# Kernel optimization log

Measured on AMD Instinct MI355X. Metric: run time of the kernel, lower is better.

Reference implementation:

```python
import jax, jax.numpy as jnp
import numpy as np

N_NODES = 20000
N_EDGES = 320000
IN_F = 256
OUT_F = 256
EDGE_F = 256


def _mlp2(x, W1, b1, W2, b2):
    # MLPLayers(2, [d_in, 2*d_in, d_out]) = Linear -> ReLU -> Linear
    return jax.nn.relu(x @ W1 + b1) @ W2 + b2


def setup_inputs() -> dict:
    key = jax.random.key(0)
    ks = jax.random.split(key, 12)

    def lin(k, fan_in, shape):
        bound = 1.0 / np.sqrt(fan_in)
        return jax.random.uniform(k, shape, jnp.float32, -bound, bound)

    node_feat = jax.random.normal(ks[0], (N_NODES, IN_F), jnp.float32)
    edge_feat = jax.random.normal(ks[1], (N_EDGES, EDGE_F), jnp.float32)
    src = jax.random.randint(ks[2], (N_EDGES,), 0, N_NODES, jnp.int32)
    dst = jax.random.randint(ks[3], (N_EDGES,), 0, N_NODES, jnp.int32)

    # edge_mlp: edge_feats -> 2*edge_feats -> in_feats
    We1 = lin(ks[4], EDGE_F, (EDGE_F, 2 * EDGE_F))
    be1 = lin(ks[5], EDGE_F, (2 * EDGE_F,))
    We2 = lin(ks[6], 2 * EDGE_F, (2 * EDGE_F, IN_F))
    be2 = lin(ks[7], 2 * EDGE_F, (IN_F,))
    # node mlp: in_feats -> 2*in_feats -> out_feats
    Wn1 = lin(ks[8], IN_F, (IN_F, 2 * IN_F))
    bn1 = lin(ks[9], IN_F, (2 * IN_F,))
    Wn2 = lin(ks[10], 2 * IN_F, (2 * IN_F, OUT_F))
    bn2 = lin(ks[11], 2 * IN_F, (OUT_F,))
    eps = jnp.zeros((1,), jnp.float32)

    return {"node_feat": node_feat, "edge_feat": edge_feat, "src": src, "dst": dst,
            "We1": We1, "be1": be1, "We2": We2, "be2": be2,
            "Wn1": Wn1, "bn1": bn1, "Wn2": Wn2, "bn2": bn2, "eps": eps}


def reference(node_feat, edge_feat, src, dst, We1, be1, We2, be2, Wn1, bn1, Wn2, bn2, eps):
    e = _mlp2(edge_feat, We1, be1, We2, be2)            # [E, IN_F]
    msg = jax.nn.relu(node_feat[src] + e)               # gather-add-relu
    out_h = jax.ops.segment_sum(msg, dst, num_segments=N_NODES)  # [N, IN_F]
    out = _mlp2((1.0 + eps[0]) * node_feat + out_h, Wn1, bn1, Wn2, bn2)
    return out
```

## Files before the change

kernel.cpp:

```cpp
#include <hip/hip_runtime.h>
#include <hip/hip_bf16.h>

#define NN  20000
#define NE  320000
#define FIN 256
#define FH  512

typedef __attribute__((ext_vector_type(8))) short bf16x8;
typedef __attribute__((ext_vector_type(4))) float f32x4;
typedef __attribute__((ext_vector_type(4))) unsigned short u16x4;
typedef __attribute__((ext_vector_type(4))) unsigned int u32x4;

static __device__ __forceinline__ unsigned short f2b(float f) {
    union { float f; unsigned int i; } v; v.f = f;
    return (unsigned short)((v.i + 0x7fffu + ((v.i >> 16) & 1u)) >> 16);
}
static __device__ __forceinline__ f32x4 mfma16(bf16x8 a, bf16x8 b, f32x4 c) {
    return __builtin_amdgcn_mfma_f32_16x16x32_bf16(a, b, c, 0, 0, 0);
}
static __device__ __forceinline__ unsigned int cvtpk(float lo, float hi) {
    union { __hip_bfloat162 h; unsigned int u; } v;
    v.h = __float22bfloat162_rn(float2{lo, hi});
    return v.u;
}
static __device__ __forceinline__ u16x4 pack4(float a, float b, float c, float d) {
    union { u16x4 s; unsigned int u[2]; } v;
    v.u[0] = cvtpk(a, b); v.u[1] = cvtpk(c, d);
    return v.s;
}
static __device__ __forceinline__ bf16x8 cvt8(f32x4 a, f32x4 b) {
    u32x4 t;
    t[0] = cvtpk(a[0], a[1]);
    t[1] = cvtpk(a[2], a[3]);
    t[2] = cvtpk(b[0], b[1]);
    t[3] = cvtpk(b[2], b[3]);
    return __builtin_bit_cast(bf16x8, t);
}

__global__ void prep_weights(const float* __restrict__ We1, const float* __restrict__ We2,
                             const float* __restrict__ Wn1, const float* __restrict__ Wn2,
                             unsigned short* __restrict__ W1F, unsigned short* __restrict__ W2F,
                             unsigned short* __restrict__ Wn1F, unsigned short* __restrict__ Wn2F) {
    const int b = blockIdx.x;
    const int m = b >> 8;
    const int f = b & 255;
    const float* src; unsigned short* dst; int N, K;
    if      (m == 0) { src = We1; dst = W1F;  N = 512; K = 256; }
    else if (m == 1) { src = We2; dst = W2F;  N = 256; K = 512; }
    else if (m == 2) { src = Wn1; dst = Wn1F; N = 512; K = 256; }
    else             { src = Wn2; dst = Wn2F; N = 256; K = 512; }
    const int KB  = K >> 5;
    const int nf  = f / KB, ks = f % KB;
    const int l   = threadIdx.x;
    const int quad = l >> 4, ln = l & 15;
    const int n  = nf * 16 + ln;
    const int k0 = ks * 32 + quad * 8;
    f32x4 a, c;
    #pragma unroll
    for (int j = 0; j < 4; ++j) {
        a[j] = src[(size_t)(k0 + j) * N + n];
        c[j] = src[(size_t)(k0 + 4 + j) * N + n];
    }
    *(bf16x8*)(dst + ((size_t)f * 64 + l) * 8) = cvt8(a, c);
}

__global__ void hist_dst(const int* __restrict__ dstI, int* __restrict__ cnt) {
    int e = blockIdx.x * 256 + threadIdx.x;
    if (e < NE) atomicAdd(&cnt[dstI[e]], 1);
}

__global__ void scan_excl(const int* __restrict__ cnt, int* __restrict__ cursor) {
    __shared__ int c[NN];
    __shared__ int s[1024];
    const int t = threadIdx.x;
    for (int i = t; i < NN; i += 1024) c[i] = cnt[i];
    __syncthreads();
    const int lo = t * 20;
    const int hi = (lo + 20 < NN) ? lo + 20 : NN;
    int sum = 0;
    for (int i = lo; i < hi; ++i) sum += c[i];
    s[t] = sum;
    __syncthreads();
    for (int off = 1; off < 1024; off <<= 1) {
        int v = (t >= off) ? s[t - off] : 0;
        __syncthreads();
        s[t] += v;
        __syncthreads();
    }
    int base = (t > 0) ? s[t - 1] : 0;
    for (int i = lo; i < hi; ++i) { int cv = c[i]; c[i] = base; base += cv; }
    __syncthreads();
    for (int i = t; i < NN; i += 1024) cursor[i] = c[i];
}

__global__ void scatter_perm(const int* __restrict__ dstI,
                             int* __restrict__ cursor, int* __restrict__ perm) {
    int e = blockIdx.x * 256 + threadIdx.x;
    if (e < NE) {
        int pos = atomicAdd(&cursor[dstI[e]], 1);
        perm[pos] = e;
    }
}

__global__ void __launch_bounds__(512, 4)
gine_edge(const float* __restrict__ edge_feat,
          const float* __restrict__ node_feat,
          const int* __restrict__ srcI,
          const int* __restrict__ dstI,
          const int* __restrict__ perm,
          const unsigned short* __restrict__ W1F,
          const float* __restrict__ b1,
          const unsigned short* __restrict__ W2F,
          const float* __restrict__ b2,
          float* __restrict__ out_h)
{
    __shared__ union {
        unsigned short Xs[64 * 264];
        unsigned short Hs[64 * 512];
        float          Msg[64 * 260];
    } sh;
    __shared__ int snS[64], dnS[64];

    const int tid  = threadIdx.x;
    const int wave = tid >> 6;
    const int lane = tid & 63;
    const int quad = lane >> 4;
    const int ln   = lane & 15;
    const int bs   = (blockIdx.x & 7) * 625 + (blockIdx.x >> 3);
    const int e0   = bs * 64;

    #pragma unroll
    for (int it = 0; it < 4; ++it) {
        const int chunk = tid + it * 512;
        const int row = chunk >> 5;
        const int c8  = (chunk & 31) << 3;
        const int e   = perm[e0 + row];
        const float* p = edge_feat + (size_t)e * FIN + c8;
        f32x4 o0 = *(const f32x4*)(p);
        f32x4 o1 = *(const f32x4*)(p + 4);
        *(bf16x8*)(&sh.Xs[row * 264 + c8]) = cvt8(o0, o1);
    }
    if (tid < 64) {
        const int e = perm[e0 + tid];
        snS[tid] = srcI[e];
        dnS[tid] = dstI[e];
    }
    __syncthreads();

    f32x4 zero4 = {0.f, 0.f, 0.f, 0.f};
    f32x4 acc1[4][4];
    #pragma unroll
    for (int nt = 0; nt < 4; ++nt)
        #pragma unroll
        for (int et = 0; et < 4; ++et) acc1[nt][et] = zero4;

    __builtin_amdgcn_s_setprio(1);
    #pragma unroll
    for (int ks = 0; ks < 8; ++ks) {
        bf16x8 w[4], x[4];
        #pragma unroll
        for (int nt = 0; nt < 4; ++nt)
            w[nt] = *(const bf16x8*)(W1F + (((wave * 4 + nt) * 8 + ks) * 64 + lane) * 8);
        #pragma unroll
        for (int et = 0; et < 4; ++et)
            x[et] = *(const bf16x8*)(&sh.Xs[(et * 16 + ln) * 264 + quad * 8 + ks * 32]);
        #pragma unroll
        for (int nt = 0; nt < 4; ++nt)
            #pragma unroll
            for (int et = 0; et < 4; ++et)
                acc1[nt][et] = mfma16(w[nt], x[et], acc1[nt][et]);
    }
    __builtin_amdgcn_s_setprio(0);
    __syncthreads();

    #pragma unroll
    for (int nt = 0; nt < 4; ++nt) {
        const int n0 = wave * 64 + nt * 16 + quad * 4;
        const f32x4 b4 = *(const f32x4*)(b1 + n0);
        #pragma unroll
        for (int et = 0; et < 4; ++et) {
            const int edge = et * 16 + ln;
            u16x4 p = pack4(fmaxf(acc1[nt][et][0] + b4[0], 0.f),
                            fmaxf(acc1[nt][et][1] + b4[1], 0.f),
                            fmaxf(acc1[nt][et][2] + b4[2], 0.f),
                            fmaxf(acc1[nt][et][3] + b4[3], 0.f));
            *(u16x4*)(&sh.Hs[(edge << 9) + (((n0 >> 3) ^ (edge & 7)) << 3) + (n0 & 7)]) = p;
        }
    }
    __syncthreads();

    f32x4 nfr[2][4];
    #pragma unroll
    for (int nt = 0; nt < 2; ++nt) {
        const int n0 = wave * 32 + nt * 16 + quad * 4;
        #pragma unroll
        for (int et = 0; et < 4; ++et) {
            const int sn = snS[et * 16 + ln];
            nfr[nt][et] = *(const f32x4*)(node_feat + (size_t)sn * FIN + n0);
        }
    }

    f32x4 acc2[2][4];
    #pragma unroll
    for (int nt = 0; nt < 2; ++nt)
        #pragma unroll
        for (int et = 0; et < 4; ++et) acc2[nt][et] = zero4;

    __builtin_amdgcn_s_setprio(1);
    #pragma unroll
    for (int ks = 0; ks < 16; ++ks) {
        const int kb = ks * 4 + quad;
        bf16x8 w[2], h[4];
        #pragma unroll
        for (int nt = 0; nt < 2; ++nt)
            w[nt] = *(const bf16x8*)(W2F + (((wave * 2 + nt) * 16 + ks) * 64 + lane) * 8);
        #pragma unroll
        for (int et = 0; et < 4; ++et) {
            const int edge = et * 16 + ln;
            h[et] = *(const bf16x8*)(&sh.Hs[(edge << 9) + ((kb ^ (edge & 7)) << 3)]);
        }
        #pragma unroll
        for (int nt = 0; nt < 2; ++nt)
            #pragma unroll
            for (int et = 0; et < 4; ++et)
                acc2[nt][et] = mfma16(w[nt], h[et], acc2[nt][et]);
    }
    __builtin_amdgcn_s_setprio(0);
    __syncthreads();

    #pragma unroll
    for (int nt = 0; nt < 2; ++nt) {
        const int n0 = wave * 32 + nt * 16 + quad * 4;
        const f32x4 b4 = *(const f32x4*)(b2 + n0);
        #pragma unroll
        for (int et = 0; et < 4; ++et) {
            const int edge = et * 16 + ln;
            f32x4 m;
            #pragma unroll
            for (int r = 0; r < 4; ++r)
                m[r] = fmaxf(nfr[nt][et][r] + acc2[nt][et][r] + b4[r], 0.f);
            *(f32x4*)(&sh.Msg[edge * 260 + n0]) = m;
        }
    }
    __syncthreads();

    {
        const int col  = tid & 255;
        const int half = tid >> 8;
        const int rA   = half * 32;
        const int dF = dnS[rA], dL = dnS[rA + 31];
        float run = sh.Msg[rA * 260 + col];
        int cur = dF;
        #pragma unroll 4
        for (int row = rA + 1; row < rA + 32; ++row) {
            const int d = dnS[row];
            if (d != cur) {
                if (cur == dF || cur == dL)
                    atomicAdd(&out_h[(size_t)cur * FIN + col], run);
                else
                    out_h[(size_t)cur * FIN + col] = run;
                run = 0.f;
                cur = d;
            }
            run += sh.Msg[row * 260 + col];
        }
        atomicAdd(&out_h[(size_t)cur * FIN + col], run);
    }
}

__global__ void __launch_bounds__(512, 4)
gine_node(const float* __restrict__ node_feat,
          const float* __restrict__ out_h,
          const unsigned short* __restrict__ W1F,
          const float* __restrict__ b1,
          const unsigned short* __restrict__ W2F,
          const float* __restrict__ b2,
          const float* __restrict__ eps,
          float* __restrict__ out)
{
    __shared__ union {
        unsigned short Xs[64 * 264];
        unsigned short Hs[64 * 512];
    } sh;

    const int tid  = threadIdx.x;
    const int wave = tid >> 6;
    const int lane = tid & 63;
    const int quad = lane >> 4;
    const int ln   = lane & 15;
    const int n0b  = blockIdx.x * 64;
    const float epsv = 1.0f + eps[0];

    #pragma unroll
    for (int it = 0; it < 4; ++it) {
        const int chunk = tid + it * 512;
        const int row = chunk >> 5;
        const int c8  = (chunk & 31) << 3;
        const int g   = n0b + row;
        bf16x8 pack = {0, 0, 0, 0, 0, 0, 0, 0};
        if (g < NN) {
            const float* pn = node_feat + (size_t)g * FIN + c8;
            const float* ph = out_h + (size_t)g * FIN + c8;
            f32x4 n0v = *(const f32x4*)(pn);
            f32x4 n1v = *(const f32x4*)(pn + 4);
            f32x4 h0v = *(const f32x4*)(ph);
            f32x4 h1v = *(const f32x4*)(ph + 4);
            f32x4 a, b;
            #pragma unroll
            for (int j = 0; j < 4; ++j) {
                a[j] = epsv * n0v[j] + h0v[j];
                b[j] = epsv * n1v[j] + h1v[j];
            }
            pack = cvt8(a, b);
        }
        *(bf16x8*)(&sh.Xs[row * 264 + c8]) = pack;
    }
    __syncthreads();

    f32x4 zero4 = {0.f, 0.f, 0.f, 0.f};
    f32x4 acc1[4][4];
    #pragma unroll
    for (int nt = 0; nt < 4; ++nt)
        #pragma unroll
        for (int et = 0; et < 4; ++et) acc1[nt][et] = zero4;

    __builtin_amdgcn_s_setprio(1);
    #pragma unroll
    for (int ks = 0; ks < 8; ++ks) {
        bf16x8 w[4], xv[4];
        #pragma unroll
        for (int nt = 0; nt < 4; ++nt)
            w[nt] = *(const bf16x8*)(W1F + (((wave * 4 + nt) * 8 + ks) * 64 + lane) * 8);
        #pragma unroll
        for (int et = 0; et < 4; ++et)
            xv[et] = *(const bf16x8*)(&sh.Xs[(et * 16 + ln) * 264 + quad * 8 + ks * 32]);
        #pragma unroll
        for (int nt = 0; nt < 4; ++nt)
            #pragma unroll
            for (int et = 0; et < 4; ++et)
                acc1[nt][et] = mfma16(w[nt], xv[et], acc1[nt][et]);
    }
    __builtin_amdgcn_s_setprio(0);
    __syncthreads();

    #pragma unroll
    for (int nt = 0; nt < 4; ++nt) {
        const int n0 = wave * 64 + nt * 16 + quad * 4;
        const f32x4 b4 = *(const f32x4*)(b1 + n0);
        #pragma unroll
        for (int et = 0; et < 4; ++et) {
            const int edge = et * 16 + ln;
            u16x4 p = pack4(fmaxf(acc1[nt][et][0] + b4[0], 0.f),
                            fmaxf(acc1[nt][et][1] + b4[1], 0.f),
                            fmaxf(acc1[nt][et][2] + b4[2], 0.f),
                            fmaxf(acc1[nt][et][3] + b4[3], 0.f));
            *(u16x4*)(&sh.Hs[(edge << 9) + (((n0 >> 3) ^ (edge & 7)) << 3) + (n0 & 7)]) = p;
        }
    }
    __syncthreads();

    f32x4 acc2[2][4];
    #pragma unroll
    for (int nt = 0; nt < 2; ++nt)
        #pragma unroll
        for (int et = 0; et < 4; ++et) acc2[nt][et] = zero4;

    __builtin_amdgcn_s_setprio(1);
    #pragma unroll
    for (int ks = 0; ks < 16; ++ks) {
        const int kb = ks * 4 + quad;
        bf16x8 w[2], h[4];
        #pragma unroll
        for (int nt = 0; nt < 2; ++nt)
            w[nt] = *(const bf16x8*)(W2F + (((wave * 2 + nt) * 16 + ks) * 64 + lane) * 8);
        #pragma unroll
        for (int et = 0; et < 4; ++et) {
            const int edge = et * 16 + ln;
            h[et] = *(const bf16x8*)(&sh.Hs[(edge << 9) + ((kb ^ (edge & 7)) << 3)]);
        }
        #pragma unroll
        for (int nt = 0; nt < 2; ++nt)
            #pragma unroll
            for (int et = 0; et < 4; ++et)
                acc2[nt][et] = mfma16(w[nt], h[et], acc2[nt][et]);
    }
    __builtin_amdgcn_s_setprio(0);

    #pragma unroll
    for (int nt = 0; nt < 2; ++nt) {
        const int n0 = wave * 32 + nt * 16 + quad * 4;
        const f32x4 b4 = *(const f32x4*)(b2 + n0);
        #pragma unroll
        for (int et = 0; et < 4; ++et) {
            const int g = n0b + et * 16 + ln;
            if (g < NN) {
                f32x4 o;
                #pragma unroll
                for (int r = 0; r < 4; ++r)
                    o[r] = acc2[nt][et][r] + b4[r];
                *(f32x4*)(out + (size_t)g * FIN + n0) = o;
            }
        }
    }
}

extern "C" void kernel_launch(void* const* d_in, const int* in_sizes, int n_in,
                              void* d_out, int out_size, void* d_ws, size_t ws_size,
                              hipStream_t stream) {
    const float* node_feat = (const float*)d_in[0];
    const float* edge_feat = (const float*)d_in[1];
    const int* srcI = (const int*)d_in[2];
    const int* dstI = (const int*)d_in[3];
    const float* We1 = (const float*)d_in[4];
    const float* be1 = (const float*)d_in[5];
    const float* We2 = (const float*)d_in[6];
    const float* be2 = (const float*)d_in[7];
    const float* Wn1 = (const float*)d_in[8];
    const float* bn1 = (const float*)d_in[9];
    const float* Wn2 = (const float*)d_in[10];
    const float* bn2 = (const float*)d_in[11];
    const float* eps = (const float*)d_in[12];

    char* ws = (char*)d_ws;
    float* out_h = (float*)ws;
    unsigned short* W1F  = (unsigned short*)(ws + 20480000);
    unsigned short* W2F  = W1F + 131072;
    unsigned short* Wn1F = W2F + 131072;
    unsigned short* Wn2F = Wn1F + 131072;
    int* cnt    = (int*)(ws + 20480000 + 4 * 262144);
    int* cursor = cnt + NN;
    int* perm   = cursor + NN;

    hipMemsetAsync(out_h, 0, (size_t)NN * FIN * sizeof(float), stream);
    hipMemsetAsync(cnt, 0, NN * sizeof(int), stream);

    prep_weights<<<1024, 64, 0, stream>>>(We1, We2, Wn1, Wn2, W1F, W2F, Wn1F, Wn2F);

    hist_dst<<<(NE + 255) / 256, 256, 0, stream>>>(dstI, cnt);
    scan_excl<<<1, 1024, 0, stream>>>(cnt, cursor);
    scatter_perm<<<(NE + 255) / 256, 256, 0, stream>>>(dstI, cursor, perm);

    gine_edge<<<NE / 64, 512, 0, stream>>>(edge_feat, node_feat, srcI, dstI,
                                           perm, W1F, be1, W2F, be2, out_h);
    gine_node<<<(NN + 63) / 64, 512, 0, stream>>>(node_feat, out_h, Wn1F, bn1,
                                                  Wn2F, bn2, eps, (float*)d_out);
}
```

Measured before the change: 820.8 us.

## Overlap second half of edge-feature load with first-layer MFMA via async LDS loads

Splits the edge-feature tile load in the edge kernel into two halves. The first 128 columns are loaded through registers, converted to bf16 and stored, while the second half is fetched asynchronously straight into an extra fp32 LDS buffer with global_load_lds. The first four K-steps of the first GEMM run while that fetch is in flight, then the second half is converted and the last four K-steps run. This adds 32 KB of shared memory to the union, which may lower occupancy, and adds an extra barrier. The gine_node argument edit is a no-op.

```diff
diff --git a/kernel.cpp b/kernel.cpp
--- a/kernel.cpp
+++ b/kernel.cpp
@@ -35,6 +35,14 @@
     t[2] = cvtpk(b[0], b[1]);
     t[3] = cvtpk(b[2], b[3]);
     return __builtin_bit_cast(bf16x8, t);
+}
+static __device__ __forceinline__ void gll16(const float* g, const float* l) {
+    __builtin_amdgcn_global_load_lds(
+        (const __attribute__((address_space(1))) unsigned int*)g,
+        (__attribute__((address_space(3))) unsigned int*)l, 16, 0, 0);
+}
+static __device__ __forceinline__ void bar_lgkm() {
+    asm volatile("s_waitcnt lgkmcnt(0)\ns_barrier" ::: "memory");
 }
 
 __global__ void prep_weights(const float* __restrict__ We1, const float* __restrict__ We2,
@@ -115,7 +123,10 @@
           float* __restrict__ out_h)
 {
     __shared__ union {
-        unsigned short Xs[64 * 264];
+        struct {
+            unsigned short Xs[64 * 264];
+            float          Xf[8192];
+        } x;
         unsigned short Hs[64 * 512];
         float          Msg[64 * 260];
     } sh;
@@ -129,23 +140,37 @@
     const int bs   = (blockIdx.x & 7) * 625 + (blockIdx.x >> 3);
     const int e0   = bs * 64;
 
-    #pragma unroll
-    for (int it = 0; it < 4; ++it) {
-        const int chunk = tid + it * 512;
-        const int row = chunk >> 5;
-        const int c8  = (chunk & 31) << 3;
-        const int e   = perm[e0 + row];
-        const float* p = edge_feat + (size_t)e * FIN + c8;
-        f32x4 o0 = *(const f32x4*)(p);
-        f32x4 o1 = *(const f32x4*)(p + 4);
-        *(bf16x8*)(&sh.Xs[row * 264 + c8]) = cvt8(o0, o1);
+    f32x4 a0[2], b0[2];
+    #pragma unroll
+    for (int i = 0; i < 2; ++i) {
+        const int c = tid + i * 512;
+        const int row = c >> 4;
+        const int off = (c & 15) << 3;
+        const float* p = edge_feat + (size_t)perm[e0 + row] * FIN + off;
+        a0[i] = *(const f32x4*)p;
+        b0[i] = *(const f32x4*)(p + 4);
+    }
+    #pragma unroll
+    for (int i = 0; i < 4; ++i) {
+        const int g   = (wave * 4 + i) * 64 + lane;
+        const int row = g >> 5;
+        const int o4  = (g & 31) << 2;
+        const float* p = edge_feat + (size_t)perm[e0 + row] * FIN + 128 + o4;
+        gll16(p, &sh.x.Xf[(wave * 4 + i) * 256]);
     }
     if (tid < 64) {
         const int e = perm[e0 + tid];
         snS[tid] = srcI[e];
         dnS[tid] = dstI[e];
     }
-    __syncthreads();
+    #pragma unroll
+    for (int i = 0; i < 2; ++i) {
+        const int c = tid + i * 512;
+        const int row = c >> 4;
+        const int off = (c & 15) << 3;
+        *(bf16x8*)(&sh.x.Xs[row * 264 + off]) = cvt8(a0[i], b0[i]);
+    }
+    bar_lgkm();
 
     f32x4 zero4 = {0.f, 0.f, 0.f, 0.f};
     f32x4 acc1[4][4];
@@ -156,14 +181,45 @@
 
     __builtin_amdgcn_s_setprio(1);
     #pragma unroll
-    for (int ks = 0; ks < 8; ++ks) {
+    for (int ks = 0; ks < 4; ++ks) {
         bf16x8 w[4], x[4];
         #pragma unroll
         for (int nt = 0; nt < 4; ++nt)
             w[nt] = *(const bf16x8*)(W1F + (((wave * 4 + nt) * 8 + ks) * 64 + lane) * 8);
         #pragma unroll
         for (int et = 0; et < 4; ++et)
-            x[et] = *(const bf16x8*)(&sh.Xs[(et * 16 + ln) * 264 + quad * 8 + ks * 32]);
+            x[et] = *(const bf16x8*)(&sh.x.Xs[(et * 16 + ln) * 264 + quad * 8 + ks * 32]);
+        #pragma unroll
+        for (int nt = 0; nt < 4; ++nt)
+            #pragma unroll
+            for (int et = 0; et < 4; ++et)
+                acc1[nt][et] = mfma16(w[nt], x[et], acc1[nt][et]);
+    }
+    __builtin_amdgcn_s_setprio(0);
+
+    asm volatile("s_waitcnt vmcnt(0)" ::: "memory");
+    #pragma unroll
+    for (int i = 0; i < 2; ++i) {
+        const int cl  = i * 64 + lane;
+        const int row = wave * 8 + (cl >> 4);
+        const int off = (cl & 15) << 3;
+        const float* pf = &sh.x.Xf[row * 128 + off];
+        f32x4 a = *(const f32x4*)pf;
+        f32x4 b = *(const f32x4*)(pf + 4);
+        *(bf16x8*)(&sh.x.Xs[row * 264 + 128 + off]) = cvt8(a, b);
+    }
+    bar_lgkm();
+
+    __builtin_amdgcn_s_setprio(1);
+    #pragma unroll
+    for (int ks = 4; ks < 8; ++ks) {
+        bf16x8 w[4], x[4];
+        #pragma unroll
+        for (int nt = 0; nt < 4; ++nt)
+            w[nt] = *(const bf16x8*)(W1F + (((wave * 4 + nt) * 8 + ks) * 64 + lane) * 8);
+        #pragma unroll
+        for (int et = 0; et < 4; ++et)
+            x[et] = *(const bf16x8*)(&sh.x.Xs[(et * 16 + ln) * 264 + quad * 8 + ks * 32]);
         #pragma unroll
         for (int nt = 0; nt < 4; ++nt)
             #pragma unroll
@@ -442,6 +498,6 @@
 
     gine_edge<<<NE / 64, 512, 0, stream>>>(edge_feat, node_feat, srcI, dstI,
                                            perm, W1F, be1, W2F, be2, out_h);
-    gine_node<<<(NN + 63) / 64, 512, 0, stream>>>(node_feat, out_h, Wn1F, bn1,
+    gine_node<<<(NN + 63) / 64, 512, 0, stream>>>(node_feat, out_h, W1F == Wn1F ? Wn1F : Wn1F, bn1,
                                                   Wn2F, bn2, eps, (float*)d_out);
 }
```

Measured after the change: 821.8 us. No clear change (+0.1%).

## Fuse weight prep, histogram, scan and scatter into one persistent kernel

Applied to the files above, without the earlier changes.

Replaces four small preprocessing kernels (weight repack, dst histogram, single-block scan, permutation scatter) with one 256-block persistent kernel that uses software grid barriers between phases. The scan becomes a distributed per-block partial sum plus a 256-entry block-level scan instead of a single 1024-thread block. This is meant to remove launch gaps and the serial single-block scan. In exchange it relies on all 256 blocks of 1024 threads being co-resident for the spin barriers, which risks deadlock if they are not.

```diff
diff --git a/kernel.cpp b/kernel.cpp
--- a/kernel.cpp
+++ b/kernel.cpp
@@ -37,66 +37,93 @@
     return __builtin_bit_cast(bf16x8, t);
 }
 
-__global__ void prep_weights(const float* __restrict__ We1, const float* __restrict__ We2,
-                             const float* __restrict__ Wn1, const float* __restrict__ Wn2,
-                             unsigned short* __restrict__ W1F, unsigned short* __restrict__ W2F,
-                             unsigned short* __restrict__ Wn1F, unsigned short* __restrict__ Wn2F) {
-    const int b = blockIdx.x;
-    const int m = b >> 8;
-    const int f = b & 255;
-    const float* src; unsigned short* dst; int N, K;
-    if      (m == 0) { src = We1; dst = W1F;  N = 512; K = 256; }
-    else if (m == 1) { src = We2; dst = W2F;  N = 256; K = 512; }
-    else if (m == 2) { src = Wn1; dst = Wn1F; N = 512; K = 256; }
-    else             { src = Wn2; dst = Wn2F; N = 256; K = 512; }
-    const int KB  = K >> 5;
-    const int nf  = f / KB, ks = f % KB;
-    const int l   = threadIdx.x;
-    const int quad = l >> 4, ln = l & 15;
-    const int n  = nf * 16 + ln;
-    const int k0 = ks * 32 + quad * 8;
-    f32x4 a, c;
-    #pragma unroll
-    for (int j = 0; j < 4; ++j) {
-        a[j] = src[(size_t)(k0 + j) * N + n];
-        c[j] = src[(size_t)(k0 + 4 + j) * N + n];
-    }
-    *(bf16x8*)(dst + ((size_t)f * 64 + l) * 8) = cvt8(a, c);
-}
-
-__global__ void hist_dst(const int* __restrict__ dstI, int* __restrict__ cnt) {
-    int e = blockIdx.x * 256 + threadIdx.x;
-    if (e < NE) atomicAdd(&cnt[dstI[e]], 1);
-}
-
-__global__ void scan_excl(const int* __restrict__ cnt, int* __restrict__ cursor) {
-    __shared__ int c[NN];
-    __shared__ int s[1024];
-    const int t = threadIdx.x;
-    for (int i = t; i < NN; i += 1024) c[i] = cnt[i];
-    __syncthreads();
-    const int lo = t * 20;
-    const int hi = (lo + 20 < NN) ? lo + 20 : NN;
-    int sum = 0;
-    for (int i = lo; i < hi; ++i) sum += c[i];
-    s[t] = sum;
-    __syncthreads();
-    for (int off = 1; off < 1024; off <<= 1) {
-        int v = (t >= off) ? s[t - off] : 0;
+static __device__ __forceinline__ void gridbar(int* ctr, int nblk) {
+    __syncthreads();
+    if (threadIdx.x == 0) {
+        __threadfence();
+        atomicAdd(ctr, 1);
+        while (atomicAdd(ctr, 0) < nblk) __builtin_amdgcn_s_sleep(1);
+    }
+    __syncthreads();
+}
+
+__global__ void __launch_bounds__(1024, 1)
+prep_all(const float* __restrict__ We1, const float* __restrict__ We2,
+         const float* __restrict__ Wn1, const float* __restrict__ Wn2,
+         const int* __restrict__ dstI,
+         unsigned short* __restrict__ W1F, unsigned short* __restrict__ W2F,
+         unsigned short* __restrict__ Wn1F, unsigned short* __restrict__ Wn2F,
+         int* __restrict__ cnt, int* __restrict__ gbar,
+         int* __restrict__ bsum, int* __restrict__ bbase,
+         int* __restrict__ cursor, int* __restrict__ perm)
+{
+    const int tid = threadIdx.x;
+    const int b   = blockIdx.x;
+
+    {
+        const int gw = b * 16 + (tid >> 6);
+        if (gw < 1024) {
+            const int m = gw >> 8, f = gw & 255;
+            const float* src; unsigned short* dst; int N, K;
+            if      (m == 0) { src = We1; dst = W1F;  N = 512; K = 256; }
+            else if (m == 1) { src = We2; dst = W2F;  N = 256; K = 512; }
+            else if (m == 2) { src = Wn1; dst = Wn1F; N = 512; K = 256; }
+            else             { src = Wn2; dst = Wn2F; N = 256; K = 512; }
+            const int KB = K >> 5;
+            const int nf = f / KB, ks = f % KB;
+            const int l  = tid & 63;
+            const int n  = nf * 16 + (l & 15);
+            const int k0 = ks * 32 + (l >> 4) * 8;
+            f32x4 a, c;
+            #pragma unroll
+            for (int j = 0; j < 4; ++j) {
+                a[j] = src[(size_t)(k0 + j) * N + n];
+                c[j] = src[(size_t)(k0 + 4 + j) * N + n];
+            }
+            *(bf16x8*)(dst + ((size_t)f * 64 + l) * 8) = cvt8(a, c);
+        }
+    }
+
+    for (int e = b * 1024 + tid; e < NE; e += 256 * 1024)
+        atomicAdd(&cnt[dstI[e]], 1);
+    gridbar(gbar + 0, 256);
+
+    __shared__ int ls[80];
+    __shared__ int ss[256];
+    const int lo = b * 80;
+    const int hi = (lo + 80 <= NN) ? 80 : ((NN > lo) ? NN - lo : 0);
+    if (tid < hi) ls[tid] = atomicAdd(&cnt[lo + tid], 0);
+    __syncthreads();
+    if (tid == 0) {
+        int s = 0;
+        for (int i = 0; i < hi; ++i) s += ls[i];
+        atomicExch(&bsum[b], s);
+    }
+    gridbar(gbar + 1, 256);
+
+    if (b == 0) {
+        int v = 0;
+        if (tid < 256) { v = atomicAdd(&bsum[tid], 0); ss[tid] = v; }
         __syncthreads();
-        s[t] += v;
-        __syncthreads();
-    }
-    int base = (t > 0) ? s[t - 1] : 0;
-    for (int i = lo; i < hi; ++i) { int cv = c[i]; c[i] = base; base += cv; }
-    __syncthreads();
-    for (int i = t; i < NN; i += 1024) cursor[i] = c[i];
-}
-
-__global__ void scatter_perm(const int* __restrict__ dstI,
-                             int* __restrict__ cursor, int* __restrict__ perm) {
-    int e = blockIdx.x * 256 + threadIdx.x;
-    if (e < NE) {
+        for (int off = 1; off < 256; off <<= 1) {
+            int t = 0;
+            if (tid < 256 && tid >= off) t = ss[tid - off];
+            __syncthreads();
+            if (tid < 256) ss[tid] += t;
+            __syncthreads();
+        }
+        if (tid < 256) atomicExch(&bbase[tid], ss[tid] - v);
+    }
+    gridbar(gbar + 2, 256);
+
+    if (tid == 0 && hi > 0) {
+        int base = atomicAdd(&bbase[b], 0);
+        for (int i = 0; i < hi; ++i) { int c = ls[i]; cursor[lo + i] = base; base += c; }
+        __threadfence();
+    }
+    gridbar(gbar + 3, 256);
+
+    for (int e = b * 1024 + tid; e < NE; e += 256 * 1024) {
         int pos = atomicAdd(&cursor[dstI[e]], 1);
         perm[pos] = e;
     }
@@ -428,17 +455,18 @@
     unsigned short* Wn1F = W2F + 131072;
     unsigned short* Wn2F = Wn1F + 131072;
     int* cnt    = (int*)(ws + 20480000 + 4 * 262144);
-    int* cursor = cnt + NN;
+    int* gbar   = cnt + NN;
+    int* bsum   = gbar + 8;
+    int* bbase  = bsum + 256;
+    int* cursor = bbase + 256;
     int* perm   = cursor + NN;
 
     hipMemsetAsync(out_h, 0, (size_t)NN * FIN * sizeof(float), stream);
-    hipMemsetAsync(cnt, 0, NN * sizeof(int), stream);
-
-    prep_weights<<<1024, 64, 0, stream>>>(We1, We2, Wn1, Wn2, W1F, W2F, Wn1F, Wn2F);
-
-    hist_dst<<<(NE + 255) / 256, 256, 0, stream>>>(dstI, cnt);
-    scan_excl<<<1, 1024, 0, stream>>>(cnt, cursor);
-    scatter_perm<<<(NE + 255) / 256, 256, 0, stream>>>(dstI, cursor, perm);
+    hipMemsetAsync(cnt, 0, (NN + 8) * sizeof(int), stream);
+
+    prep_all<<<256, 1024, 0, stream>>>(We1, We2, Wn1, Wn2, dstI,
+                                       W1F, W2F, Wn1F, Wn2F,
+                                       cnt, gbar, bsum, bbase, cursor, perm);
 
     gine_edge<<<NE / 64, 512, 0, stream>>>(edge_feat, node_feat, srcI, dstI,
                                            perm, W1F, be1, W2F, be2, out_h);
```

Result: slower. 860.8 us (+4.9%).
